# Kernel optimization log

Hardware: AMD Instinct MI355X
Metric: run time of the kernel (lower is better)

The kernel has to match this reference:

```python
import jax, jax.numpy as jnp
import numpy as np

B, T, E, H = 2, 2048, 1024, 16
D = E // H            # head dim = 64
ROT = D // 2          # rotary_dim = 32 (only first half of head dim is rotated)
THETA = 10000.0


def _rope(x):
    # x: (B, H, T, D). Faithful to rotary_embedding_torch.rotate_queries_or_keys
    # with dim=ROT: rotate first ROT features, interleaved-pair style, pass rest.
    t = x.shape[-2]
    inv = 1.0 / (THETA ** (jnp.arange(0, ROT, 2, dtype=jnp.float32) / ROT))   # (ROT//2,)
    freqs = jnp.arange(t, dtype=jnp.float32)[:, None] * inv[None, :]          # (T, ROT//2)
    freqs = jnp.repeat(freqs, 2, axis=-1)                                      # (T, ROT)
    cos, sin = jnp.cos(freqs), jnp.sin(freqs)
    xr, xp = x[..., :ROT], x[..., ROT:]
    p = xr.reshape(*xr.shape[:-1], ROT // 2, 2)
    rot = jnp.stack((-p[..., 1], p[..., 0]), axis=-1).reshape(xr.shape)
    return jnp.concatenate([xr * cos + rot * sin, xp], axis=-1)


def setup_inputs() -> dict:
    key = jax.random.key(0)
    k1, k2, k3 = jax.random.split(key, 3)
    query = jax.random.normal(k1, (B, T, E), dtype=jnp.float32)
    inputs = {
        "query": query,
        "key": query,            # ignored (cross_attention=False)
        "value": query,          # ignored
        "padding_mask": jnp.ones((B, T), dtype=bool),
        "in_proj_weight": jax.random.uniform(k2, (3 * E, E), dtype=jnp.float32),
        "out_proj_weight": jax.random.normal(k3, (E, E), dtype=jnp.float32) * (E ** -0.5),
    }
    return inputs


def reference(query, key, value, padding_mask, in_proj_weight, out_proj_weight):
    # cross_attention=False: key/value are overwritten by query
    key = query
    value = query
    q = query @ in_proj_weight[:E].T
    k = key @ in_proj_weight[E:2 * E].T
    v = value @ in_proj_weight[2 * E:].T
    # NOTE: raw reshape (B,T,E)->(B,H,T,D), exactly as in the torch module
    q = q.reshape(B, H, T, D)
    k = k.reshape(B, H, T, D)
    v = v.reshape(B, H, T, D)
    q = _rope(q)
    k = _rope(k)   # causal self-attention path: rotate keys too
    causal = jnp.tril(jnp.ones((T, T), dtype=bool))                 # (T, T)
    mask = causal[None, None] & padding_mask[:, None, None, :]      # (B,1,T,T) -> broadcast over H
    scores = jnp.einsum("bhqd,bhkd->bhqk", q, k) / jnp.sqrt(jnp.float32(D))
    scores = jnp.where(mask, scores, -jnp.inf)
    attn = jax.nn.softmax(scores, axis=-1)
    x = jnp.einsum("bhqk,bhkd->bhqd", attn, v)
    x = x.reshape(B, T, E)      # raw reshape back, as in torch
    return x @ out_proj_weight.T
```

## Files before the change

### kernel.cpp

```cpp
#include <hip/hip_runtime.h>
#include <stdint.h>

#define T_ 2048
#define E_ 1024

typedef __attribute__((ext_vector_type(8))) __bf16 bf16x8;
typedef __attribute__((ext_vector_type(4))) float f32x4;

__device__ __forceinline__ void gload_lds16(const void* g, void* l) {
  __builtin_amdgcn_global_load_lds(
      (const __attribute__((address_space(1))) unsigned int*)g,
      (__attribute__((address_space(3))) unsigned int*)l, 16, 0, 0);
}

__global__ __launch_bounds__(256) void k_prep(const float4* __restrict__ q,
                                              ushort4* __restrict__ xh,
                                              ushort4* __restrict__ xl,
                                              const float4* __restrict__ win,
                                              ushort4* __restrict__ whh,
                                              ushort4* __restrict__ whl,
                                              const float4* __restrict__ wout,
                                              ushort4* __restrict__ wob,
                                              float2* __restrict__ cs) {
  const int b = blockIdx.x, tid = threadIdx.x;
  if (b < 7168) {
    const float4* src;
    ushort4 *hi, *lo;
    int i;
    if (b < 4096) { src = q; hi = xh; lo = xl; i = b * 256 + tid; }
    else          { src = win; hi = whh; lo = whl; i = (b - 4096) * 256 + tid; }
    float4 x = src[i];
    float xs[4] = {x.x, x.y, x.z, x.w};
    union { __bf16 bb[4]; ushort4 u; } H, L;
#pragma unroll
    for (int jj = 0; jj < 4; ++jj) {
      __bf16 h = (__bf16)xs[jj];
      H.bb[jj] = h;
      L.bb[jj] = (__bf16)(xs[jj] - (float)h);
    }
    hi[i] = H.u;
    lo[i] = L.u;
  } else if (b < 8192) {
    int i = (b - 7168) * 256 + tid;
    float4 x = wout[i];
    float xs[4] = {x.x, x.y, x.z, x.w};
    union { __bf16 bb[4]; ushort4 u; } H;
#pragma unroll
    for (int jj = 0; jj < 4; ++jj) H.bb[jj] = (__bf16)xs[jj];
    wob[i] = H.u;
  } else {
    int i = (b - 8192) * 256 + tid;
    int t = i >> 4, f = i & 15;
    double inv = pow(10000.0, -(double)f / 16.0);
    double ang = (double)t * inv;
    cs[i] = make_float2((float)cos(ang), (float)sin(ang));
  }
}

__global__ __launch_bounds__(256) void k_proj(const __bf16* __restrict__ xh,
                                              const __bf16* __restrict__ xl,
                                              const __bf16* __restrict__ whh,
                                              const __bf16* __restrict__ whl,
                                              const float2* __restrict__ cs,
                                              __bf16* __restrict__ qhi,
                                              __bf16* __restrict__ qlo,
                                              __bf16* __restrict__ khi,
                                              __bf16* __restrict__ klo,
                                              __bf16* __restrict__ v16t) {
  __shared__ __align__(16) __bf16 AsH[128 * 64];
  __shared__ __align__(16) __bf16 BsH[128 * 64];
  __shared__ __align__(16) __bf16 AsL[128 * 64];
  __shared__ __align__(16) __bf16 BsL[128 * 64];
  const int tid = threadIdx.x, lane = tid & 63, w = tid >> 6;
  const int g = lane >> 4, d = lane & 15;
  const int lr8 = lane >> 3;
  const int swz8 = ((lane & 7) ^ lr8) * 8;
  const int rsl = d & 7;
  const int K = 1024;

  if (blockIdx.x < 512) {
    const int bi = blockIdx.x;
    const int bx = (bi >> 3) & 15;
    const int by = ((bi & 7) << 2) | ((bi >> 7) & 3);
    const int wm = w >> 1, wn = w & 1;
    const int m0 = by * 128, n0 = bx * 128;

    f32x4 acc[4][4];
#pragma unroll
    for (int i = 0; i < 4; ++i)
#pragma unroll
      for (int j = 0; j < 4; ++j) acc[i][j] = (f32x4)(0.0f);

    for (int k0 = 0; k0 < K; k0 += 64) {
      __syncthreads();
#pragma unroll
      for (int c = 0; c < 4; ++c) {
        const int rr = c * 32 + w * 8 + lr8;
        const int ldo = (c * 32 + w * 8) * 64;
        gload_lds16(xh + (size_t)(m0 + rr) * K + k0 + swz8, &AsH[ldo]);
        gload_lds16(xl + (size_t)(m0 + rr) * K + k0 + swz8, &AsL[ldo]);
        gload_lds16(whh + (size_t)(n0 + rr) * K + k0 + swz8, &BsH[ldo]);
        gload_lds16(whl + (size_t)(n0 + rr) * K + k0 + swz8, &BsL[ldo]);
      }
      __syncthreads();
#pragma unroll
      for (int k2 = 0; k2 < 2; ++k2) {
        const int sl = ((k2 * 4 + g) ^ rsl) * 8;
        bf16x8 bh[4], bl[4];
#pragma unroll
        for (int j = 0; j < 4; ++j) {
          const int r = wn * 64 + j * 16 + d;
          bh[j] = *(const bf16x8*)&BsH[r * 64 + sl];
          bl[j] = *(const bf16x8*)&BsL[r * 64 + sl];
        }
#pragma unroll
        for (int i = 0; i < 4; ++i) {
          const int r = wm * 64 + i * 16 + d;
          const bf16x8 ahf = *(const bf16x8*)&AsH[r * 64 + sl];
          const bf16x8 alf = *(const bf16x8*)&AsL[r * 64 + sl];
#pragma unroll
          for (int j = 0; j < 4; ++j) {
            acc[i][j] = __builtin_amdgcn_mfma_f32_16x16x32_bf16(ahf, bh[j], acc[i][j], 0, 0, 0);
            acc[i][j] = __builtin_amdgcn_mfma_f32_16x16x32_bf16(alf, bh[j], acc[i][j], 0, 0, 0);
            acc[i][j] = __builtin_amdgcn_mfma_f32_16x16x32_bf16(ahf, bl[j], acc[i][j], 0, 0, 0);
          }
        }
      }
    }

#pragma unroll
    for (int i = 0; i < 4; ++i) {
      const int rbase = m0 + (w >> 1) * 64 + i * 16 + g * 4;
#pragma unroll
      for (int j = 0; j < 4; ++j) {
        const int col = n0 + (w & 1) * 64 + j * 16 + d;
#pragma unroll
        for (int r = 0; r < 4; ++r) {
          const float vv = acc[i][j][r];
          const int row = rbase + r;
          const float xp = __shfl_xor(vv, 1);
          const int which = col >> 10;
          const int cl = col & 1023;
          const int d2 = cl & 63;
          const int t2 = (row & 127) * 16 + (cl >> 6);
          float y;
          if (d2 < 32) {
            const float2 cse = cs[t2 * 16 + (d2 >> 1)];
            y = (d2 & 1) ? (vv * cse.x + xp * cse.y) : (vv * cse.x - xp * cse.y);
          } else {
            y = vv;
          }
          if (which == 0) y *= 0.18033688011112042f;
          const __bf16 hi = (__bf16)y;
          const __bf16 lo = (__bf16)(y - (float)hi);
          const size_t off = (size_t)row * 1024 + cl;
          (which ? khi : qhi)[off] = hi;
          (which ? klo : qlo)[off] = lo;
        }
      }
    }
  } else {
    const int bi = blockIdx.x - 512;
    const int bx = (bi >> 3) & 7;
    const int by = ((bi & 7) << 3) | ((bi >> 6) & 7);
    const int m0 = by * 64, n0 = bx * 128;
    const __bf16* Bv = whh + (size_t)2048 * 1024;

    f32x4 acc[4][2];
#pragma unroll
    for (int i = 0; i < 4; ++i)
#pragma unroll
      for (int j = 0; j < 2; ++j) acc[i][j] = (f32x4)(0.0f);

    for (int k0 = 0; k0 < K; k0 += 64) {
      __syncthreads();
#pragma unroll
      for (int c = 0; c < 2; ++c) {
        const int rr = c * 32 + w * 8 + lr8;
        gload_lds16(xh + (size_t)(m0 + rr) * K + k0 + swz8, &AsH[(c * 32 + w * 8) * 64]);
      }
#pragma unroll
      for (int c = 0; c < 4; ++c) {
        const int rr = c * 32 + w * 8 + lr8;
        gload_lds16(Bv + (size_t)(n0 + rr) * K + k0 + swz8, &BsH[(c * 32 + w * 8) * 64]);
      }
      __syncthreads();
#pragma unroll
      for (int k2 = 0; k2 < 2; ++k2) {
        const int sl = ((k2 * 4 + g) ^ rsl) * 8;
        bf16x8 bh[2], ah[4];
#pragma unroll
        for (int j = 0; j < 2; ++j)
          bh[j] = *(const bf16x8*)&BsH[(w * 32 + j * 16 + d) * 64 + sl];
#pragma unroll
        for (int i = 0; i < 4; ++i)
          ah[i] = *(const bf16x8*)&AsH[(i * 16 + d) * 64 + sl];
#pragma unroll
        for (int i = 0; i < 4; ++i)
#pragma unroll
          for (int j = 0; j < 2; ++j)
            acc[i][j] = __builtin_amdgcn_mfma_f32_16x16x32_bf16(ah[i], bh[j], acc[i][j], 0, 0, 0);
      }
    }

#pragma unroll
    for (int i = 0; i < 4; ++i) {
      const int rbase = m0 + i * 16 + g * 4;
#pragma unroll
      for (int j = 0; j < 2; ++j) {
        const int col = n0 + w * 32 + j * 16 + d;
#pragma unroll
        for (int r = 0; r < 4; ++r) {
          const int row = rbase + r;
          const int p = row >> 7;
          const int tp = ((row & 127) << 4) | (col >> 6);
          const int dp = col & 63;
          v16t[((size_t)p * 64 + dp) * 2048 + tp] = (__bf16)acc[i][j][r];
        }
      }
    }
  }
}

__global__ __launch_bounds__(256) void k_gemmout(const __bf16* __restrict__ Ah,
                                                 const __bf16* __restrict__ Bh,
                                                 float* __restrict__ C32) {
  __shared__ __align__(16) __bf16 As[32 * 64];
  __shared__ __align__(16) __bf16 Bs[128 * 64];
  const int bi = blockIdx.x;
  const int bx = (bi >> 3) & 7;
  const int by = ((bi & 7) << 4) | (bi >> 6);
  const int tid = threadIdx.x, lane = tid & 63, w = tid >> 6;
  const int g = lane >> 4, d = lane & 15;
  const int m0 = by * 32, n0 = bx * 128;
  const int K = 1024, N = 1024;

  f32x4 acc[2][2];
#pragma unroll
  for (int i = 0; i < 2; ++i)
#pragma unroll
    for (int j = 0; j < 2; ++j) acc[i][j] = (f32x4)(0.0f);

  const int lr8 = lane >> 3;
  const int swz8 = ((lane & 7) ^ lr8) * 8;
  const int rsl = d & 7;

  for (int k0 = 0; k0 < K; k0 += 64) {
    __syncthreads();
    gload_lds16(Ah + (size_t)(m0 + w * 8 + lr8) * K + k0 + swz8, &As[(w * 8) * 64]);
#pragma unroll
    for (int c = 0; c < 4; ++c) {
      const int rr = c * 32 + w * 8 + lr8;
      gload_lds16(Bh + (size_t)(n0 + rr) * K + k0 + swz8, &Bs[(c * 32 + w * 8) * 64]);
    }
    __syncthreads();
#pragma unroll
    for (int k2 = 0; k2 < 2; ++k2) {
      const int sl = ((k2 * 4 + g) ^ rsl) * 8;
      bf16x8 bh[2], ah[2];
#pragma unroll
      for (int j = 0; j < 2; ++j)
        bh[j] = *(const bf16x8*)&Bs[(w * 32 + j * 16 + d) * 64 + sl];
#pragma unroll
      for (int i = 0; i < 2; ++i)
        ah[i] = *(const bf16x8*)&As[(i * 16 + d) * 64 + sl];
#pragma unroll
      for (int i = 0; i < 2; ++i)
#pragma unroll
        for (int j = 0; j < 2; ++j)
          acc[i][j] = __builtin_amdgcn_mfma_f32_16x16x32_bf16(ah[i], bh[j], acc[i][j], 0, 0, 0);
    }
  }

#pragma unroll
  for (int i = 0; i < 2; ++i) {
    const int rbase = m0 + i * 16 + g * 4;
#pragma unroll
    for (int j = 0; j < 2; ++j) {
      const int col = n0 + w * 32 + j * 16 + d;
#pragma unroll
      for (int r = 0; r < 4; ++r)
        C32[(size_t)(rbase + r) * N + col] = acc[i][j][r];
    }
  }
}

__global__ __launch_bounds__(512, 4) void k_attn(const __bf16* __restrict__ qhi,
                                                 const __bf16* __restrict__ qlo,
                                                 const __bf16* __restrict__ khi,
                                                 const __bf16* __restrict__ klo,
                                                 const __bf16* __restrict__ v16t,
                                                 __bf16* __restrict__ x16,
                                                 float* __restrict__ po,
                                                 float* __restrict__ pm,
                                                 float* __restrict__ pl_) {
  __shared__ __align__(16) __bf16 KH[2][64 * 64];
  __shared__ __align__(16) __bf16 KL[2][64 * 64];
  __shared__ __align__(16) __bf16 VT[2][64 * 64];
  __shared__ __align__(16) __bf16 PL[8][16 * 72];

  const int bi = blockIdx.x;
  const int b = (bi >> 3) & 15;
  const int panel = (bi & 7) | (((bi >> 7) & 3) << 3);
  const int u0 = 9 * b;
  int qtA = 0;
  while (2 * (qtA + 1) * (qtA + 2) <= u0) ++qtA;
  const int cumA = 2 * qtA * (qtA + 1);
  const int cumB = 2 * (qtA + 1) * (qtA + 2);
  const int jloA = u0 - cumA;
  const bool two = (u0 + 9 > cumB);
  const int jhiA = two ? (cumB - 1 - cumA) : (u0 + 8 - cumA);
  const int jhiB = u0 + 8 - cumB;

  const int tid = threadIdx.x, lane = tid & 63, w = tid >> 6;
  const int g = lane >> 4, d = lane & 15;
  const size_t hb = (size_t)panel * T_ * 64;

  const int kr = tid >> 3, kc = tid & 7;
  const int swz = (kc ^ (kr & 7)) * 8;
  const __bf16* kB = khi + hb;
  const __bf16* lB = klo + hb;
  const __bf16* vB = v16t + (size_t)panel * (64 * T_);

#define STAGE(j, bb)                                                        \
  {                                                                         \
    gload_lds16(kB + (size_t)((j) * 64 + kr) * 64 + swz, &KH[bb][w * 512]); \
    gload_lds16(lB + (size_t)((j) * 64 + kr) * 64 + swz, &KL[bb][w * 512]); \
    gload_lds16(vB + (size_t)kr * T_ + (j) * 64 + swz, &VT[bb][w * 512]);   \
  }

  int cur = 0;
  STAGE(jloA, 0);

  for (int seg = 0; seg < 2; ++seg) {
    if (seg && !two) break;
    const int qt = qtA + seg;
    const int jlo = seg ? 0 : jloA;
    const int jhi = seg ? jhiB : jhiA;
    const int q0 = qt << 8;

    bf16x8 qh[2][2], ql[2][2];
#pragma unroll
    for (int rb = 0; rb < 2; ++rb) {
      const int rbi = w * 2 + rb;
      const size_t qrow = hb + (size_t)(q0 + rbi * 16 + d) * 64;
      qh[rb][0] = *(const bf16x8*)&qhi[qrow + g * 8];
      qh[rb][1] = *(const bf16x8*)&qhi[qrow + 32 + g * 8];
      ql[rb][0] = *(const bf16x8*)&qlo[qrow + g * 8];
      ql[rb][1] = *(const bf16x8*)&qlo[qrow + 32 + g * 8];
    }

    f32x4 o[2][4];
#pragma unroll
    for (int rb = 0; rb < 2; ++rb)
#pragma unroll
      for (int i = 0; i < 4; ++i) o[rb][i] = (f32x4)(0.0f);
    float m_[2] = {-__builtin_inff(), -__builtin_inff()};
    float l_[2] = {0.0f, 0.0f};

    for (int j = jlo; j <= jhi; ++j) {
      __syncthreads();
      if (j < jhi) {
        STAGE(j + 1, cur ^ 1);
      } else if (!seg && two) {
        STAGE(0, cur ^ 1);
      }

#pragma unroll
      for (int rb = 0; rb < 2; ++rb) {
        const int rbi = w * 2 + rb;
        const int qrow0 = q0 + rbi * 16;
        if (j * 64 > qrow0 + 15) continue;

        f32x4 s[4];
        __builtin_amdgcn_s_setprio(1);
#pragma unroll
        for (int f = 0; f < 4; ++f) {
          f32x4 accs = (f32x4)(0.0f);
          const int colr = f * 16 + d;
#pragma unroll
          for (int ds = 0; ds < 2; ++ds) {
            const int slot = ((ds * 4 + g) ^ (colr & 7)) * 8;
            const bf16x8 kf = *(const bf16x8*)&KH[cur][colr * 64 + slot];
            const bf16x8 lf = *(const bf16x8*)&KL[cur][colr * 64 + slot];
            accs = __builtin_amdgcn_mfma_f32_16x16x32_bf16(kf, qh[rb][ds], accs, 0, 0, 0);
            accs = __builtin_amdgcn_mfma_f32_16x16x32_bf16(kf, ql[rb][ds], accs, 0, 0, 0);
            accs = __builtin_amdgcn_mfma_f32_16x16x32_bf16(lf, qh[rb][ds], accs, 0, 0, 0);
          }
          s[f] = accs;
        }
        __builtin_amdgcn_s_setprio(0);

        if (j * 64 + 63 > qrow0) {
          const int qq = qrow0 + d;
#pragma unroll
          for (int f = 0; f < 4; ++f)
#pragma unroll
            for (int r = 0; r < 4; ++r) {
              const int kv = j * 64 + f * 16 + g * 4 + r;
              if (kv > qq) s[f][r] = -30000.0f;
            }
        }

        float pmax = fmaxf(fmaxf(s[0][0], s[0][1]), fmaxf(s[0][2], s[0][3]));
#pragma unroll
        for (int f = 1; f < 4; ++f)
          pmax = fmaxf(pmax, fmaxf(fmaxf(s[f][0], s[f][1]), fmaxf(s[f][2], s[f][3])));
        pmax = fmaxf(pmax, __shfl_xor(pmax, 16));
        pmax = fmaxf(pmax, __shfl_xor(pmax, 32));

        if (!__all(pmax - m_[rb] <= 11.5f)) {
          const float mnew = fmaxf(m_[rb], pmax);
          const float fac = exp2f(m_[rb] - mnew);
          m_[rb] = mnew;
          float facr[4];
#pragma unroll
          for (int r = 0; r < 4; ++r)
            facr[r] = __shfl(fac, (lane & 48) | (g * 4 + r));
#pragma unroll
          for (int ni = 0; ni < 4; ++ni)
#pragma unroll
            for (int r = 0; r < 4; ++r) o[rb][ni][r] *= facr[r];
          l_[rb] *= fac;
        }

        float sum = 0.0f;
#pragma unroll
        for (int f = 0; f < 4; ++f) {
          union { __bf16 bb[4]; ushort4 u4; } pk;
#pragma unroll
          for (int r = 0; r < 4; ++r) {
            const float pv = exp2f(s[f][r] - m_[rb]);
            sum += pv;
            pk.bb[r] = (__bf16)pv;
          }
          *(ushort4*)&PL[w][d * 72 + f * 16 + g * 4] = pk.u4;
        }
        sum += __shfl_xor(sum, 16);
        sum += __shfl_xor(sum, 32);
        l_[rb] += sum;

        __builtin_amdgcn_s_setprio(1);
#pragma unroll
        for (int ks = 0; ks < 2; ++ks) {
          const bf16x8 pa = *(const bf16x8*)&PL[w][d * 72 + ks * 32 + g * 8];
#pragma unroll
          for (int ni = 0; ni < 4; ++ni) {
            const bf16x8 vf =
                *(const bf16x8*)&VT[cur][(ni * 16 + d) * 64 + (((ks * 4 + g) ^ (d & 7)) * 8)];
            o[rb][ni] = __builtin_amdgcn_mfma_f32_16x16x32_bf16(pa, vf, o[rb][ni], 0, 0, 0);
          }
        }
        __builtin_amdgcn_s_setprio(0);
      }
      cur ^= 1;
    }

    if (jlo == 0 && jhi == 4 * qt + 3) {
#pragma unroll
      for (int rb = 0; rb < 2; ++rb) {
        const int rbi = w * 2 + rb;
        float lr[4];
#pragma unroll
        for (int r = 0; r < 4; ++r)
          lr[r] = __shfl(l_[rb], (lane & 48) | (g * 4 + r));
#pragma unroll
        for (int ni = 0; ni < 4; ++ni)
#pragma unroll
          for (int r = 0; r < 4; ++r) {
            const size_t row = hb + (size_t)(q0 + rbi * 16 + g * 4 + r) * 64;
            x16[row + ni * 16 + d] = (__bf16)(o[rb][ni][r] / lr[r]);
          }
      }
    } else {
      const int slot = panel * 23 + b + qt;
#pragma unroll
      for (int rb = 0; rb < 2; ++rb) {
        const int rbi = w * 2 + rb;
#pragma unroll
        for (int ni = 0; ni < 4; ++ni)
#pragma unroll
          for (int r = 0; r < 4; ++r) {
            const int rowin = rbi * 16 + g * 4 + r;
            po[(size_t)slot * 16384 + rowin * 64 + ni * 16 + d] = o[rb][ni][r];
          }
        if (g == 0) {
          pm[slot * 256 + rbi * 16 + d] = m_[rb];
          pl_[slot * 256 + rbi * 16 + d] = l_[rb];
        }
      }
    }
  }
#undef STAGE
}

__global__ __launch_bounds__(256) void k_combine(const float* __restrict__ po,
                                                 const float* __restrict__ pm,
                                                 const float* __restrict__ pl_,
                                                 __bf16* __restrict__ x16) {
  const int bi = blockIdx.x;
  const int p = (bi & 7) | ((bi / 3584) << 3);
  const int li = ((bi >> 3) % 448) * 256 + threadIdx.x;
  const int d = li & 63;
  const int t2 = 256 + (li >> 6);
  const int qt = t2 >> 8;
  const int rowin = t2 & 255;
  const int cq = 2 * qt * (qt + 1);
  const int nc = (cq + 4 * qt + 3) / 9 - cq / 9 + 1;
  const int s0 = p * 23 + cq / 9 + qt;
  float M = -__builtin_inff();
  for (int s = 0; s < nc; ++s) M = fmaxf(M, pm[(s0 + s) * 256 + rowin]);
  float L = 0.0f, O = 0.0f;
  for (int s = 0; s < nc; ++s) {
    const float ww = exp2f(pm[(s0 + s) * 256 + rowin] - M);
    L += pl_[(s0 + s) * 256 + rowin] * ww;
    O += po[(size_t)(s0 + s) * 16384 + rowin * 64 + d] * ww;
  }
  x16[((size_t)p * T_ + t2) * 64 + d] = (__bf16)(O / L);
}

extern "C" void kernel_launch(void* const* d_in, const int* in_sizes, int n_in,
                              void* d_out, int out_size, void* d_ws, size_t ws_size,
                              hipStream_t stream) {
  const float* query = (const float*)d_in[0];
  const float* win = (const float*)d_in[4];
  const float* wout = (const float*)d_in[5];
  float* out = (float*)d_out;

  const size_t MB = 1024 * 1024;
  const size_t KB = 1024;
  char* ws = (char*)d_ws;
  __bf16* xh = (__bf16*)(ws);
  __bf16* xl = (__bf16*)(ws + 8 * MB);
  __bf16* whh = (__bf16*)(ws + 16 * MB);
  __bf16* whl = (__bf16*)(ws + 22 * MB);
  float* po = (float*)(ws);
  __bf16* v16t = (__bf16*)(ws + 46 * MB);
  __bf16* qhi = (__bf16*)(ws + 54 * MB);
  __bf16* qlo = (__bf16*)(ws + 62 * MB);
  __bf16* khi = (__bf16*)(ws + 70 * MB);
  __bf16* klo = (__bf16*)(ws + 78 * MB);
  __bf16* wob = (__bf16*)(ws + 86 * MB);
  float* pm = (float*)(ws + 88 * MB);
  float* pl_ = (float*)(ws + 88 * MB + 768 * KB);
  float2* cs = (float2*)(ws + 89 * MB + 512 * KB);
  __bf16* x16 = (__bf16*)(ws + 54 * MB);

  k_prep<<<8320, 256, 0, stream>>>((const float4*)query, (ushort4*)xh, (ushort4*)xl,
                                   (const float4*)win, (ushort4*)whh, (ushort4*)whl,
                                   (const float4*)wout, (ushort4*)wob, cs);

  k_proj<<<1024, 256, 0, stream>>>(xh, xl, whh, whl, cs, qhi, qlo, khi, klo, v16t);

  k_attn<<<512, 512, 0, stream>>>(qhi, qlo, khi, klo, v16t, x16, po, pm, pl_);

  k_combine<<<14336, 256, 0, stream>>>(po, pm, pl_, x16);

  k_gemmout<<<1024, 256, 0, stream>>>(x16, wob, out);
}
```

Measured before the change: 186.3 us.

## Double-buffer LDS tiles in projection GEMM with 32-wide K steps

The QK and V projection GEMMs now keep two LDS buffers with a K step of 32 instead of a single buffer with a K step of 64. Global-to-LDS loads for the next step are issued right after the barrier, so they overlap the MFMA work on the current buffer, and one of the two barriers per step is removed. The swizzle pattern is adjusted for the narrower 32-element rows. In exchange there are twice as many loop iterations. Correctness relies on the async LDS loads being complete at each barrier.

```diff
diff --git a/kernel.cpp b/kernel.cpp
--- a/kernel.cpp
+++ b/kernel.cpp
@@ -67,15 +67,16 @@
                                               __bf16* __restrict__ khi,
                                               __bf16* __restrict__ klo,
                                               __bf16* __restrict__ v16t) {
-  __shared__ __align__(16) __bf16 AsH[128 * 64];
-  __shared__ __align__(16) __bf16 BsH[128 * 64];
-  __shared__ __align__(16) __bf16 AsL[128 * 64];
-  __shared__ __align__(16) __bf16 BsL[128 * 64];
+  __shared__ __align__(16) __bf16 AsH[2][128 * 32];
+  __shared__ __align__(16) __bf16 AsL[2][128 * 32];
+  __shared__ __align__(16) __bf16 BsH[2][128 * 32];
+  __shared__ __align__(16) __bf16 BsL[2][128 * 32];
   const int tid = threadIdx.x, lane = tid & 63, w = tid >> 6;
   const int g = lane >> 4, d = lane & 15;
-  const int lr8 = lane >> 3;
-  const int swz8 = ((lane & 7) ^ lr8) * 8;
-  const int rsl = d & 7;
+  const int row0 = tid >> 2;
+  const int row1 = 64 + row0;
+  const int sw32 = ((tid & 3) ^ ((tid >> 3) & 3)) * 8;
+  const int rg = (g ^ ((d >> 1) & 3)) * 8;
   const int K = 1024;
 
   if (blockIdx.x < 512) {
@@ -91,49 +92,53 @@
 #pragma unroll
       for (int j = 0; j < 4; ++j) acc[i][j] = (f32x4)(0.0f);
 
-    for (int k0 = 0; k0 < K; k0 += 64) {
+#define STAGEQK(ks_, bb)                                                                  \
+  {                                                                                       \
+    const int kk = (ks_) * 32;                                                            \
+    gload_lds16(xh + (size_t)(m0 + row0) * K + kk + sw32, &AsH[bb][w * 512]);             \
+    gload_lds16(xh + (size_t)(m0 + row1) * K + kk + sw32, &AsH[bb][2048 + w * 512]);      \
+    gload_lds16(xl + (size_t)(m0 + row0) * K + kk + sw32, &AsL[bb][w * 512]);             \
+    gload_lds16(xl + (size_t)(m0 + row1) * K + kk + sw32, &AsL[bb][2048 + w * 512]);      \
+    gload_lds16(whh + (size_t)(n0 + row0) * K + kk + sw32, &BsH[bb][w * 512]);            \
+    gload_lds16(whh + (size_t)(n0 + row1) * K + kk + sw32, &BsH[bb][2048 + w * 512]);     \
+    gload_lds16(whl + (size_t)(n0 + row0) * K + kk + sw32, &BsL[bb][w * 512]);            \
+    gload_lds16(whl + (size_t)(n0 + row1) * K + kk + sw32, &BsL[bb][2048 + w * 512]);     \
+  }
+
+    int cur = 0;
+    STAGEQK(0, 0);
+    for (int ks = 0; ks < 32; ++ks) {
       __syncthreads();
-#pragma unroll
-      for (int c = 0; c < 4; ++c) {
-        const int rr = c * 32 + w * 8 + lr8;
-        const int ldo = (c * 32 + w * 8) * 64;
-        gload_lds16(xh + (size_t)(m0 + rr) * K + k0 + swz8, &AsH[ldo]);
-        gload_lds16(xl + (size_t)(m0 + rr) * K + k0 + swz8, &AsL[ldo]);
-        gload_lds16(whh + (size_t)(n0 + rr) * K + k0 + swz8, &BsH[ldo]);
-        gload_lds16(whl + (size_t)(n0 + rr) * K + k0 + swz8, &BsL[ldo]);
-      }
-      __syncthreads();
-#pragma unroll
-      for (int k2 = 0; k2 < 2; ++k2) {
-        const int sl = ((k2 * 4 + g) ^ rsl) * 8;
-        bf16x8 bh[4], bl[4];
+      if (ks < 31) STAGEQK(ks + 1, cur ^ 1);
+      bf16x8 bh[4], bl[4];
+#pragma unroll
+      for (int j = 0; j < 4; ++j) {
+        const int r = wn * 64 + j * 16 + d;
+        bh[j] = *(const bf16x8*)&BsH[cur][r * 32 + rg];
+        bl[j] = *(const bf16x8*)&BsL[cur][r * 32 + rg];
+      }
+#pragma unroll
+      for (int i = 0; i < 4; ++i) {
+        const int r = wm * 64 + i * 16 + d;
+        const bf16x8 ahf = *(const bf16x8*)&AsH[cur][r * 32 + rg];
+        const bf16x8 alf = *(const bf16x8*)&AsL[cur][r * 32 + rg];
 #pragma unroll
         for (int j = 0; j < 4; ++j) {
-          const int r = wn * 64 + j * 16 + d;
-          bh[j] = *(const bf16x8*)&BsH[r * 64 + sl];
-          bl[j] = *(const bf16x8*)&BsL[r * 64 + sl];
-        }
-#pragma unroll
-        for (int i = 0; i < 4; ++i) {
-          const int r = wm * 64 + i * 16 + d;
-          const bf16x8 ahf = *(const bf16x8*)&AsH[r * 64 + sl];
-          const bf16x8 alf = *(const bf16x8*)&AsL[r * 64 + sl];
-#pragma unroll
-          for (int j = 0; j < 4; ++j) {
-            acc[i][j] = __builtin_amdgcn_mfma_f32_16x16x32_bf16(ahf, bh[j], acc[i][j], 0, 0, 0);
-            acc[i][j] = __builtin_amdgcn_mfma_f32_16x16x32_bf16(alf, bh[j], acc[i][j], 0, 0, 0);
-            acc[i][j] = __builtin_amdgcn_mfma_f32_16x16x32_bf16(ahf, bl[j], acc[i][j], 0, 0, 0);
-          }
-        }
-      }
-    }
+          acc[i][j] = __builtin_amdgcn_mfma_f32_16x16x32_bf16(ahf, bh[j], acc[i][j], 0, 0, 0);
+          acc[i][j] = __builtin_amdgcn_mfma_f32_16x16x32_bf16(alf, bh[j], acc[i][j], 0, 0, 0);
+          acc[i][j] = __builtin_amdgcn_mfma_f32_16x16x32_bf16(ahf, bl[j], acc[i][j], 0, 0, 0);
+        }
+      }
+      cur ^= 1;
+    }
+#undef STAGEQK
 
 #pragma unroll
     for (int i = 0; i < 4; ++i) {
-      const int rbase = m0 + (w >> 1) * 64 + i * 16 + g * 4;
+      const int rbase = m0 + wm * 64 + i * 16 + g * 4;
 #pragma unroll
       for (int j = 0; j < 4; ++j) {
-        const int col = n0 + (w & 1) * 64 + j * 16 + d;
+        const int col = n0 + wn * 64 + j * 16 + d;
 #pragma unroll
         for (int r = 0; r < 4; ++r) {
           const float vv = acc[i][j][r];
@@ -172,36 +177,34 @@
 #pragma unroll
       for (int j = 0; j < 2; ++j) acc[i][j] = (f32x4)(0.0f);
 
-    for (int k0 = 0; k0 < K; k0 += 64) {
+#define STAGEV(ks_, bb)                                                                   \
+  {                                                                                       \
+    const int kk = (ks_) * 32;                                                            \
+    gload_lds16(xh + (size_t)(m0 + row0) * K + kk + sw32, &AsH[bb][w * 512]);             \
+    gload_lds16(Bv + (size_t)(n0 + row0) * K + kk + sw32, &BsH[bb][w * 512]);             \
+    gload_lds16(Bv + (size_t)(n0 + row1) * K + kk + sw32, &BsH[bb][2048 + w * 512]);      \
+  }
+
+    int cur = 0;
+    STAGEV(0, 0);
+    for (int ks = 0; ks < 32; ++ks) {
       __syncthreads();
-#pragma unroll
-      for (int c = 0; c < 2; ++c) {
-        const int rr = c * 32 + w * 8 + lr8;
-        gload_lds16(xh + (size_t)(m0 + rr) * K + k0 + swz8, &AsH[(c * 32 + w * 8) * 64]);
-      }
-#pragma unroll
-      for (int c = 0; c < 4; ++c) {
-        const int rr = c * 32 + w * 8 + lr8;
-        gload_lds16(Bv + (size_t)(n0 + rr) * K + k0 + swz8, &BsH[(c * 32 + w * 8) * 64]);
-      }
-      __syncthreads();
-#pragma unroll
-      for (int k2 = 0; k2 < 2; ++k2) {
-        const int sl = ((k2 * 4 + g) ^ rsl) * 8;
-        bf16x8 bh[2], ah[4];
+      if (ks < 31) STAGEV(ks + 1, cur ^ 1);
+      bf16x8 bh[2], ah[4];
+#pragma unroll
+      for (int j = 0; j < 2; ++j)
+        bh[j] = *(const bf16x8*)&BsH[cur][(w * 32 + j * 16 + d) * 32 + rg];
+#pragma unroll
+      for (int i = 0; i < 4; ++i)
+        ah[i] = *(const bf16x8*)&AsH[cur][(i * 16 + d) * 32 + rg];
+#pragma unroll
+      for (int i = 0; i < 4; ++i)
 #pragma unroll
         for (int j = 0; j < 2; ++j)
-          bh[j] = *(const bf16x8*)&BsH[(w * 32 + j * 16 + d) * 64 + sl];
-#pragma unroll
-        for (int i = 0; i < 4; ++i)
-          ah[i] = *(const bf16x8*)&AsH[(i * 16 + d) * 64 + sl];
-#pragma unroll
-        for (int i = 0; i < 4; ++i)
-#pragma unroll
-          for (int j = 0; j < 2; ++j)
-            acc[i][j] = __builtin_amdgcn_mfma_f32_16x16x32_bf16(ah[i], bh[j], acc[i][j], 0, 0, 0);
-      }
-    }
+          acc[i][j] = __builtin_amdgcn_mfma_f32_16x16x32_bf16(ah[i], bh[j], acc[i][j], 0, 0, 0);
+      cur ^= 1;
+    }
+#undef STAGEV
 
 #pragma unroll
     for (int i = 0; i < 4; ++i) {
```

New measurement: 200.2 us. 1.07x slower.
